# Kernel tuning notes

Measured on AMD Instinct MI355X. Metric: run time of the kernel, lower is better.

Reference implementation:

```python
import jax, jax.numpy as jnp
import numpy as np

B, S, D, DFF, E, TOPK = 4, 2048, 1024, 4096, 8, 2


def setup_inputs() -> dict:
    key = jax.random.key(0)
    ks = jax.random.split(key, 7)
    scale_r = 1.0 / np.sqrt(D)
    scale_1 = 1.0 / np.sqrt(D)
    scale_2 = 1.0 / np.sqrt(DFF)
    return {
        "x": jax.random.normal(ks[0], (B, S, D), dtype=jnp.float32),
        "Wr": jax.random.normal(ks[1], (D, E), dtype=jnp.float32) * scale_r,
        "br": jnp.zeros((E,), dtype=jnp.float32),
        "W1": jax.random.normal(ks[2], (E, D, DFF), dtype=jnp.float32) * scale_1,
        "b1": jnp.zeros((E, DFF), dtype=jnp.float32),
        "W2": jax.random.normal(ks[3], (E, DFF, D), dtype=jnp.float32) * scale_2,
        "b2": jnp.zeros((E, D), dtype=jnp.float32),
    }


def reference(x, Wr, br, W1, b1, W2, b2):
    # Router: per-token logits over experts. [B,S,E]
    router_logits = jnp.einsum("bsd,de->bse", x, Wr) + br
    # top-k expert selection, softmax over the k selected logits (matches
    # torch.topk + F.softmax(dim=-1) on the topk values).
    topk_w, topk_idx = jax.lax.top_k(router_logits, TOPK)  # [B,S,K]
    topk_w = jax.nn.softmax(topk_w, axis=-1)
    # Dense per-expert gates: gates[b,s,e] = sum_k topk_w[b,s,k] * [idx==e]
    one_hot = jax.nn.one_hot(topk_idx, E, dtype=x.dtype)  # [B,S,K,E]
    gates = jnp.einsum("bsk,bske->bse", topk_w, one_hot)  # [B,S,E]
    # Per-expert FFN compute + weighted scatter-add combine.
    out = jnp.zeros_like(x)
    for e in range(E):  # small fixed loop over experts
        h = jax.nn.gelu(jnp.einsum("bsd,df->bsf", x, W1[e]) + b1[e])
        y = jnp.einsum("bsf,fd->bsd", h, W2[e]) + b2[e]
        out = out + gates[:, :, e, None] * y
    return out
```

## Files before the change

kernel.cpp:

```cpp
#include <hip/hip_runtime.h>
#include <cstdio>
#include <cstdint>

#define TOKENS 8192
#define DMODEL 1024
#define DFF    4096
#define NEXP   8
#define TCAP   8192
#define ROWS   16384

typedef __attribute__((ext_vector_type(8))) short short8;
typedef __attribute__((ext_vector_type(4))) float f32x4;

__device__ __forceinline__ unsigned short f2bf(float f){
  unsigned u = __builtin_bit_cast(unsigned, f);
  u += 0x7FFFu + ((u >> 16) & 1u);
  return (unsigned short)(u >> 16);
}

__device__ __forceinline__ void async16(void* lds, const void* g){
  __builtin_amdgcn_global_load_lds((const __attribute__((address_space(1))) void*)g,
                                   (__attribute__((address_space(3))) void*)lds,
                                   16, 0, 0);
}

__device__ __forceinline__ short8 lds_read_b128(const char* p){
  short8 r;
  asm volatile("ds_read_b128 %0, %1"
               : "=v"(r)
               : "v"((const __attribute__((address_space(3))) char*)p));
  return r;
}

__device__ __forceinline__ float gelu_tanh(float x){
  float t = 0.7978845608028654f * (x + 0.044715f * x * x * x);
  float e = __expf(2.0f * t);
  float th = 1.0f - 2.0f / (e + 1.0f);
  return 0.5f * x * (1.0f + th);
}

__global__ __launch_bounds__(256) void router_kernel(
    const float* __restrict__ x, const float* __restrict__ Wr, const float* __restrict__ br,
    int* __restrict__ cnt, int* __restrict__ list,
    int* __restrict__ tk_e, int* __restrict__ tk_s, float* __restrict__ tk_g)
{
  int t = blockIdx.x * 4 + (threadIdx.x >> 6);
  int lane = threadIdx.x & 63;
  const float* xr = x + (size_t)t * DMODEL;
  float acc[8];
#pragma unroll
  for (int e = 0; e < 8; e++) acc[e] = 0.f;
#pragma unroll
  for (int j = 0; j < 16; j++){
    int d = lane + 64 * j;
    float xv = xr[d];
    const f32x4* w = (const f32x4*)(Wr + (size_t)d * 8);
    f32x4 w0 = w[0], w1 = w[1];
    acc[0] += xv * w0.x; acc[1] += xv * w0.y; acc[2] += xv * w0.z; acc[3] += xv * w0.w;
    acc[4] += xv * w1.x; acc[5] += xv * w1.y; acc[6] += xv * w1.z; acc[7] += xv * w1.w;
  }
#pragma unroll
  for (int e = 0; e < 8; e++){
    float v = acc[e];
#pragma unroll
    for (int o = 32; o > 0; o >>= 1) v += __shfl_xor(v, o, 64);
    acc[e] = v;
  }
  if (lane == 0){
    float lg[8];
#pragma unroll
    for (int e = 0; e < 8; e++) lg[e] = acc[e] + br[e];
    int i0 = 0; float v0 = lg[0];
#pragma unroll
    for (int e = 1; e < 8; e++) if (lg[e] > v0){ v0 = lg[e]; i0 = e; }
    int i1 = -1; float v1 = -3.4e38f;
#pragma unroll
    for (int e = 0; e < 8; e++) if (e != i0 && lg[e] > v1){ v1 = lg[e]; i1 = e; }
    float ew = __expf(v1 - v0);
    float w1 = ew / (1.f + ew);
    float w0 = 1.f - w1;
    int s0 = atomicAdd(&cnt[i0], 1);
    int s1 = atomicAdd(&cnt[i1], 1);
    list[i0 * TCAP + s0] = t;
    list[i1 * TCAP + s1] = t;
    tk_e[2*t]   = i0; tk_s[2*t]   = s0; tk_g[2*t]   = w0;
    tk_e[2*t+1] = i1; tk_s[2*t+1] = s1; tk_g[2*t+1] = w1;
  }
}

__global__ void scan_kernel(const int* __restrict__ cnt, int* __restrict__ off){
  if (threadIdx.x == 0 && blockIdx.x == 0){
    int o = 0;
    for (int e = 0; e < NEXP; e++){ off[e] = o; o += cnt[e]; }
    off[NEXP] = o;
  }
}

__global__ __launch_bounds__(256) void xconv_kernel(const float* __restrict__ x,
                                                    unsigned short* __restrict__ xb)
{
  size_t i = (size_t)(blockIdx.x * 256 + threadIdx.x) * 8;
  f32x4 a = *(const f32x4*)(x + i);
  f32x4 b = *(const f32x4*)(x + i + 4);
  short8 o;
  o[0]=(short)f2bf(a.x); o[1]=(short)f2bf(a.y); o[2]=(short)f2bf(a.z); o[3]=(short)f2bf(a.w);
  o[4]=(short)f2bf(b.x); o[5]=(short)f2bf(b.y); o[6]=(short)f2bf(b.z); o[7]=(short)f2bf(b.w);
  *(short8*)(xb + i) = o;
}

__global__ __launch_bounds__(256) void transpose_kernel(const float* __restrict__ src,
                                                        unsigned short* __restrict__ dst,
                                                        int R, int C)
{
  __shared__ float tile[32][33];
  int e = blockIdx.z;
  size_t ebase = (size_t)e * R * C;
  int c0 = blockIdx.x * 32;
  int r0 = blockIdx.y * 32;
  int tx = threadIdx.x & 31;
  int ty = threadIdx.x >> 5;
  const float* s = src + ebase;
  unsigned short* d = dst + ebase;
#pragma unroll
  for (int i = 0; i < 4; i++)
    tile[ty + 8*i][tx] = s[(size_t)(r0 + ty + 8*i) * C + c0 + tx];
  __syncthreads();
#pragma unroll
  for (int i = 0; i < 4; i++)
    d[(size_t)(c0 + ty + 8*i) * R + r0 + tx] = f2bf(tile[tx][ty + 8*i]);
}

template<int MODE>
__global__ __launch_bounds__(512, 1) void gemm_kernel(
    const unsigned short* __restrict__ A0, int lda,
    const int* __restrict__ list,
    const unsigned short* __restrict__ B0, int ldb, long strideBe,
    const int* __restrict__ cnt, const int* __restrict__ off,
    int K,
    unsigned short* __restrict__ hout, float* __restrict__ yout, int ldout,
    const float* __restrict__ bias, int nbase, int accum)
{
  int e = blockIdx.z;
  int cnte = cnt[e];
  int bm = blockIdx.y;
  if (bm * 256 >= cnte) return;
  int bn = blockIdx.x;
  int offe = off[e];

  __shared__ unsigned short smem[2][(256 + 256) * 64];

  int tid  = threadIdx.x;
  int lane = tid & 63;
  int wav  = tid >> 6;
  int sslot = (tid & 7) ^ ((tid >> 3) & 7);

  const unsigned short* aptr[4];
  const unsigned short* bptr[4];
  const unsigned short* Be = B0 + (size_t)e * strideBe;
#pragma unroll
  for (int c = 0; c < 4; c++){
    int r  = bm * 256 + c * 64 + (tid >> 3);
    int rr = min(r, cnte - 1);
    long arow = list ? (long)list[(size_t)e * TCAP + rr] : (long)(offe + rr);
    aptr[c] = A0 + (size_t)arow * lda + sslot * 8;
    int n = bn * 256 + c * 64 + (tid >> 3);
    bptr[c] = Be + (size_t)n * ldb + sslot * 8;
  }

  auto stage = [&](int buf, int k0){
    char* Ad = (char*)smem + (size_t)buf * 65536;
    char* Bd = Ad + 32768;
#pragma unroll
    for (int c = 0; c < 4; c++){
      async16(Ad + c * 8192 + wav * 1024, aptr[c] + k0);
      async16(Bd + c * 8192 + wav * 1024, bptr[c] + k0);
    }
  };

  f32x4 acc[8][4] = {};

  int wm = wav >> 2, wn = wav & 3;
  int l15 = lane & 15, l4 = lane >> 4;
  int swz = lane & 7;

  int NT = K >> 6;
  stage(0, 0);
  int cur = 0;
  for (int t = 0; t < NT; t++){
    if (t + 1 < NT){
      stage(cur ^ 1, (t + 1) << 6);
      asm volatile("s_waitcnt vmcnt(8)" ::: "memory");
    } else {
      asm volatile("s_waitcnt vmcnt(0)" ::: "memory");
    }
    __builtin_amdgcn_s_barrier();
    __builtin_amdgcn_sched_barrier(0);
    char* Ab = (char*)smem + (size_t)cur * 65536;
    char* Bb = Ab + 32768;
#pragma unroll
    for (int kk = 0; kk < 2; kk++){
      short8 a[8], b[4];
      int k8 = kk * 4 + l4;
      int ks = (k8 ^ swz) << 4;
#pragma unroll
      for (int m = 0; m < 8; m++){
        int row = wm * 128 + m * 16 + l15;
        a[m] = lds_read_b128(Ab + row * 128 + ks);
      }
#pragma unroll
      for (int n = 0; n < 4; n++){
        int col = wn * 64 + n * 16 + l15;
        b[n] = lds_read_b128(Bb + col * 128 + ks);
      }
      asm volatile("s_waitcnt lgkmcnt(0)" ::: "memory");
      __builtin_amdgcn_sched_barrier(0);
      __builtin_amdgcn_s_setprio(1);
#pragma unroll
      for (int m = 0; m < 8; m++)
#pragma unroll
        for (int n = 0; n < 4; n++)
          acc[m][n] = __builtin_amdgcn_mfma_f32_16x16x32_bf16(a[m], b[n], acc[m][n], 0, 0, 0);
      __builtin_amdgcn_s_setprio(0);
    }
    __builtin_amdgcn_s_barrier();
    cur ^= 1;
  }

#pragma unroll
  for (int m = 0; m < 8; m++){
#pragma unroll
    for (int n = 0; n < 4; n++){
      int coll = bn * 256 + wn * 64 + n * 16 + l15;
#pragma unroll
      for (int q = 0; q < 4; q++){
        int r = bm * 256 + wm * 128 + m * 16 + l4 * 4 + q;
        if (r < cnte){
          float v = acc[m][n][q];
          size_t orow = (size_t)(offe + r);
          if (MODE == 0){
            v += bias[(size_t)e * DFF + nbase + coll];
            v = gelu_tanh(v);
            hout[orow * (size_t)ldout + coll] = f2bf(v);
          } else {
            size_t oi = orow * (size_t)ldout + coll;
            if (accum) v += yout[oi];
            yout[oi] = v;
          }
        }
      }
    }
  }
}

__global__ __launch_bounds__(256) void combine_kernel(
    const float* __restrict__ y, const float* __restrict__ b2,
    const int* __restrict__ off, const int* __restrict__ tk_e,
    const int* __restrict__ tk_s, const float* __restrict__ tk_g,
    float* __restrict__ out)
{
  int t = blockIdx.x;
  int d = threadIdx.x * 4;
  int e0 = tk_e[2*t],  e1 = tk_e[2*t+1];
  int s0 = tk_s[2*t],  s1 = tk_s[2*t+1];
  float g0 = tk_g[2*t], g1 = tk_g[2*t+1];
  size_t r0 = (size_t)(off[e0] + s0) * DMODEL + d;
  size_t r1 = (size_t)(off[e1] + s1) * DMODEL + d;
  f32x4 v0 = *(const f32x4*)(y + r0);
  f32x4 v1 = *(const f32x4*)(y + r1);
  f32x4 c0 = *(const f32x4*)(b2 + (size_t)e0 * DMODEL + d);
  f32x4 c1 = *(const f32x4*)(b2 + (size_t)e1 * DMODEL + d);
  f32x4 o  = g0 * (v0 + c0) + g1 * (v1 + c1);
  *(f32x4*)(out + (size_t)t * DMODEL + d) = o;
}

extern "C" void kernel_launch(void* const* d_in, const int* in_sizes, int n_in,
                              void* d_out, int out_size, void* d_ws, size_t ws_size,
                              hipStream_t stream)
{
  const float* x  = (const float*)d_in[0];
  const float* Wr = (const float*)d_in[1];
  const float* br = (const float*)d_in[2];
  const float* W1 = (const float*)d_in[3];
  const float* b1 = (const float*)d_in[4];
  const float* W2 = (const float*)d_in[5];
  const float* b2 = (const float*)d_in[6];
  float* out = (float*)d_out;

  char* ws = (char*)d_ws;
  size_t o = 0;
  auto carve = [&](size_t bytes) -> char* {
    char* p = ws + o;
    o += (bytes + 255) & ~(size_t)255;
    return p;
  };
  int* cnt   = (int*)carve(NEXP * 4);
  int* off   = (int*)carve((NEXP + 1) * 4);
  int* list  = (int*)carve((size_t)NEXP * TCAP * 4);
  int* tk_e  = (int*)carve(TOKENS * 2 * 4);
  int* tk_s  = (int*)carve(TOKENS * 2 * 4);
  float* tk_g = (float*)carve(TOKENS * 2 * 4);
  unsigned short* xb  = (unsigned short*)carve((size_t)TOKENS * DMODEL * 2);
  unsigned short* W1t = (unsigned short*)carve((size_t)NEXP * DFF * DMODEL * 2);
  unsigned short* W2t = (unsigned short*)carve((size_t)NEXP * DFF * DMODEL * 2);
  float* y = (float*)carve((size_t)ROWS * DMODEL * 4);
  size_t used_base = o;

  int nchunk = 0;
  for (int nc = 1; nc <= 8; nc <<= 1){
    size_t need = used_base + (size_t)ROWS * (DFF / nc) * 2 + 256;
    if (need <= ws_size){ nchunk = nc; break; }
  }
  if (!nchunk){
    fprintf(stderr, "kernel_launch: ws too small (%zu bytes, need >= %zu)\n",
            ws_size, used_base + (size_t)ROWS * (DFF / 8) * 2 + 256);
    return;
  }
  int dffc = DFF / nchunk;
  unsigned short* h = (unsigned short*)carve((size_t)ROWS * dffc * 2);

  hipMemsetAsync(cnt, 0, NEXP * 4, stream);
  router_kernel<<<TOKENS / 4, 256, 0, stream>>>(x, Wr, br, cnt, list, tk_e, tk_s, tk_g);
  scan_kernel<<<1, 64, 0, stream>>>(cnt, off);
  xconv_kernel<<<(TOKENS * DMODEL / 8) / 256, 256, 0, stream>>>(x, xb);
  transpose_kernel<<<dim3(DFF / 32, DMODEL / 32, NEXP), 256, 0, stream>>>(W1, W1t, DMODEL, DFF);
  transpose_kernel<<<dim3(DMODEL / 32, DFF / 32, NEXP), 256, 0, stream>>>(W2, W2t, DFF, DMODEL);

  for (int c = 0; c < nchunk; c++){
    gemm_kernel<0><<<dim3(dffc / 256, TCAP / 256, NEXP), 512, 0, stream>>>(
        xb, DMODEL, list,
        W1t + (size_t)c * dffc * DMODEL, DMODEL, (long)DFF * DMODEL,
        cnt, off, DMODEL,
        h, nullptr, dffc,
        b1, c * dffc, 0);
    gemm_kernel<1><<<dim3(DMODEL / 256, TCAP / 256, NEXP), 512, 0, stream>>>(
        h, dffc, nullptr,
        W2t + (size_t)c * dffc, DFF, (long)DFF * DMODEL,
        cnt, off, dffc,
        nullptr, y, DMODEL,
        nullptr, 0, c > 0);
  }
  combine_kernel<<<TOKENS, 256, 0, stream>>>(y, b2, off, tk_e, tk_s, tk_g, out);
}
```

Before: 852.8 us.

## Split per-tile MFMA loop into four barrier-separated LDS-read/MFMA phases

```diff
diff --git a/kernel.cpp b/kernel.cpp
--- a/kernel.cpp
+++ b/kernel.cpp
@@ -197,32 +197,73 @@
     __builtin_amdgcn_sched_barrier(0);
     char* Ab = (char*)smem + (size_t)cur * 65536;
     char* Bb = Ab + 32768;
-#pragma unroll
-    for (int kk = 0; kk < 2; kk++){
-      short8 a[8], b[4];
-      int k8 = kk * 4 + l4;
-      int ks = (k8 ^ swz) << 4;
-#pragma unroll
-      for (int m = 0; m < 8; m++){
-        int row = wm * 128 + m * 16 + l15;
-        a[m] = lds_read_b128(Ab + row * 128 + ks);
-      }
-#pragma unroll
-      for (int n = 0; n < 4; n++){
-        int col = wn * 64 + n * 16 + l15;
-        b[n] = lds_read_b128(Bb + col * 128 + ks);
-      }
-      asm volatile("s_waitcnt lgkmcnt(0)" ::: "memory");
-      __builtin_amdgcn_sched_barrier(0);
-      __builtin_amdgcn_s_setprio(1);
-#pragma unroll
-      for (int m = 0; m < 8; m++)
-#pragma unroll
-        for (int n = 0; n < 4; n++)
-          acc[m][n] = __builtin_amdgcn_mfma_f32_16x16x32_bf16(a[m], b[n], acc[m][n], 0, 0, 0);
-      __builtin_amdgcn_s_setprio(0);
-    }
-    __builtin_amdgcn_s_barrier();
+    const char* Arow = Ab + (wm * 128 + l15) * 128;
+    const char* Brow = Bb + (wn * 64  + l15) * 128;
+    int ks0 = (l4 ^ swz) << 4;
+    int ks1 = ((4 + l4) ^ swz) << 4;
+
+    short8 aL[4], aH[4], b0[4], b1[4];
+
+#pragma unroll
+    for (int m = 0; m < 4; m++) aL[m] = lds_read_b128(Arow + m * 2048 + ks0);
+#pragma unroll
+    for (int n = 0; n < 4; n++) b0[n] = lds_read_b128(Brow + n * 2048 + ks0);
+    __builtin_amdgcn_s_barrier();
+    asm volatile("s_waitcnt lgkmcnt(0)" ::: "memory");
+    __builtin_amdgcn_sched_barrier(0);
+    __builtin_amdgcn_s_setprio(1);
+#pragma unroll
+    for (int m = 0; m < 4; m++)
+#pragma unroll
+      for (int n = 0; n < 4; n++)
+        acc[m][n] = __builtin_amdgcn_mfma_f32_16x16x32_bf16(aL[m], b0[n], acc[m][n], 0, 0, 0);
+    __builtin_amdgcn_s_setprio(0);
+    __builtin_amdgcn_s_barrier();
+
+#pragma unroll
+    for (int m = 0; m < 4; m++) aH[m] = lds_read_b128(Arow + 8192 + m * 2048 + ks0);
+    __builtin_amdgcn_s_barrier();
+    asm volatile("s_waitcnt lgkmcnt(0)" ::: "memory");
+    __builtin_amdgcn_sched_barrier(0);
+    __builtin_amdgcn_s_setprio(1);
+#pragma unroll
+    for (int m = 0; m < 4; m++)
+#pragma unroll
+      for (int n = 0; n < 4; n++)
+        acc[4 + m][n] = __builtin_amdgcn_mfma_f32_16x16x32_bf16(aH[m], b0[n], acc[4 + m][n], 0, 0, 0);
+    __builtin_amdgcn_s_setprio(0);
+    __builtin_amdgcn_s_barrier();
+
+#pragma unroll
+    for (int m = 0; m < 4; m++) aL[m] = lds_read_b128(Arow + m * 2048 + ks1);
+#pragma unroll
+    for (int n = 0; n < 4; n++) b1[n] = lds_read_b128(Brow + n * 2048 + ks1);
+    __builtin_amdgcn_s_barrier();
+    asm volatile("s_waitcnt lgkmcnt(0)" ::: "memory");
+    __builtin_amdgcn_sched_barrier(0);
+    __builtin_amdgcn_s_setprio(1);
+#pragma unroll
+    for (int m = 0; m < 4; m++)
+#pragma unroll
+      for (int n = 0; n < 4; n++)
+        acc[m][n] = __builtin_amdgcn_mfma_f32_16x16x32_bf16(aL[m], b1[n], acc[m][n], 0, 0, 0);
+    __builtin_amdgcn_s_setprio(0);
+    __builtin_amdgcn_s_barrier();
+
+#pragma unroll
+    for (int m = 0; m < 4; m++) aH[m] = lds_read_b128(Arow + 8192 + m * 2048 + ks1);
+    __builtin_amdgcn_s_barrier();
+    asm volatile("s_waitcnt lgkmcnt(0)" ::: "memory");
+    __builtin_amdgcn_sched_barrier(0);
+    __builtin_amdgcn_s_setprio(1);
+#pragma unroll
+    for (int m = 0; m < 4; m++)
+#pragma unroll
+      for (int n = 0; n < 4; n++)
+        acc[4 + m][n] = __builtin_amdgcn_mfma_f32_16x16x32_bf16(aH[m], b1[n], acc[4 + m][n], 0, 0, 0);
+    __builtin_amdgcn_s_setprio(0);
+    __builtin_amdgcn_s_barrier();
+
     cur ^= 1;
   }
 
```

New measurement: 873.4 us. 2.4% more time.
